# Kernel optimization log

Measured on AMD Instinct MI355X. Metric: run time of the kernel, lower is better.

The kernel has to match this reference:

```python
import jax, jax.numpy as jnp
import numpy as np

K = 6                 # color-coding parameter; K-1 message-passing steps
N = 50000             # num nodes
E = 1600000           # num edges (avg degree 32)
F = 384               # num_node_features = K * 2**K


def setup_inputs() -> dict:
    key = jax.random.key(0)
    k1, k2, k3, k4, k5 = jax.random.split(key, 5)
    s = 1.0 / np.sqrt(F)
    x = jax.random.normal(k1, (N, F), dtype=jnp.float32)
    edge_index = jax.random.randint(k2, (2, E), 0, N, dtype=jnp.int32)
    batch = jnp.zeros((N,), dtype=jnp.int32)  # unused by forward, kept for signature parity
    W_rel = jax.random.normal(k3, (F, F), dtype=jnp.float32) * s   # GraphConv lin_rel weight
    W_root = jax.random.normal(k4, (F, F), dtype=jnp.float32) * s  # GraphConv lin_root weight
    W_lin = jax.random.normal(k5, (1, F), dtype=jnp.float32) * s   # readout linear (no bias)
    return {"x": x, "edge_index": edge_index, "batch": batch,
            "W_rel": W_rel, "W_root": W_root, "W_lin": W_lin}


def reference(x, edge_index, batch, W_rel, W_root, W_lin):
    src = edge_index[0]
    dst = edge_index[1]
    # K-1 iterations of PyG GraphConv(aggr='add', bias=False) + relu:
    #   out = segment_sum(x[src] -> dst) @ W_rel^T + x @ W_root^T
    for _ in range(K - 1):
        agg = jax.ops.segment_sum(x[src], dst, num_segments=N)  # [N, F]
        x = jax.nn.relu(agg @ W_rel.T + x @ W_root.T)
    # readout: Linear(F, 1, bias=False)
    return x @ W_lin.T  # [N, 1]
```

## Files before the change

kernel.cpp:

```cpp
#include <hip/hip_runtime.h>
#include <hip/hip_bf16.h>

#define NN 50000
#define EE 1600000
#define FF 384
#define MPAD 50048
#define NITER 5
#define EPB 6250
#define BCAP 220000
#define GRP 6250

typedef unsigned int u32;
typedef unsigned short u16;
typedef __attribute__((ext_vector_type(8))) short short8;
typedef __attribute__((ext_vector_type(4))) float f32x4;

typedef const __attribute__((address_space(1))) void* gptr_t;
typedef __attribute__((address_space(3))) void* lptr_t;

__device__ __forceinline__ float bf_lo(u32 u) {
  u32 v = u << 16;
  return __builtin_bit_cast(float, v);
}
__device__ __forceinline__ float bf_hi(u32 u) {
  u32 v = u & 0xFFFF0000u;
  return __builtin_bit_cast(float, v);
}
__device__ __forceinline__ u32 f2bf(float f) {
  u32 u = __builtin_bit_cast(u32, f);
  return (u + 0x7FFFu + ((u >> 16) & 1u)) >> 16;
}
__device__ __forceinline__ u32 pack2(float lo, float hi) {
  return f2bf(lo) | (f2bf(hi) << 16);
}
__device__ __forceinline__ void load16_lds(const void* g, void* l) {
  __builtin_amdgcn_global_load_lds((gptr_t)g, (lptr_t)l, 16, 0, 0);
}

__global__ void init_bcur_kernel(int* __restrict__ bcur) {
  if (threadIdx.x < 8) bcur[threadIdx.x] = threadIdx.x * BCAP;
}

__global__ __launch_bounds__(256) void bucket_scatter_kernel(
    const int* __restrict__ src, const int* __restrict__ dst,
    int* __restrict__ bcur, int* __restrict__ es_src, int* __restrict__ es_dst) {
  __shared__ int osrc[EPB];
  __shared__ int odst[EPB];
  __shared__ int h[8], lo8[8], gbase[8], c2[8];
  const int t = threadIdx.x;
  if (t < 8) { h[t] = 0; c2[t] = 0; }
  __syncthreads();
  const int e0 = blockIdx.x * EPB;
  for (int i = t; i < EPB; i += 256) {
    int d = dst[e0 + i];
    atomicAdd(&h[d / GRP], 1);
  }
  __syncthreads();
  if (t == 0) { int r = 0; for (int b = 0; b < 8; ++b) { lo8[b] = r; r += h[b]; } }
  __syncthreads();
  if (t < 8) gbase[t] = atomicAdd(&bcur[t], h[t]);
  __syncthreads();
  for (int i = t; i < EPB; i += 256) {
    int s = src[e0 + i], d = dst[e0 + i];
    int b = d / GRP;
    int p = lo8[b] + atomicAdd(&c2[b], 1);
    osrc[p] = s; odst[p] = d;
  }
  __syncthreads();
  for (int i = t; i < EPB; i += 256) {
    int b = 0;
    while (b < 7 && i >= lo8[b + 1]) ++b;
    int g = gbase[b] + (i - lo8[b]);
    es_src[g] = osrc[i];
    es_dst[g] = odst[i];
  }
}

__global__ __launch_bounds__(256) void hist3_kernel(
    const int* __restrict__ es_dst, const int* __restrict__ bcur,
    int* __restrict__ cnt) {
  const int g = blockIdx.x & 7;
  const int sub = blockIdx.x >> 3;
  const int base = g * BCAP;
  const int n = bcur[g] - base;
  const int chunk = (n + 31) >> 5;
  const int i0 = sub * chunk;
  int i1 = i0 + chunk; if (i1 > n) i1 = n;
  for (int i = i0 + threadIdx.x; i < i1; i += 256)
    atomicAdd(&cnt[es_dst[base + i]], 1);
}

__global__ void scan_kernel(const int* __restrict__ cnt, int* __restrict__ row_start,
                            int* __restrict__ cursor) {
  __shared__ int wsum[4];
  const int CH = 196;
  int t = threadIdx.x;
  int lo = t * CH;
  int hi = lo + CH; if (hi > NN) hi = NN;
  int s = 0;
  int n4 = (hi - lo) >> 2;
  const int4* p = (const int4*)(cnt + lo);
  for (int i = 0; i < n4; ++i) { int4 c = p[i]; s += c.x + c.y + c.z + c.w; }
  int lane = t & 63, w = t >> 6;
  int v = s;
  for (int d = 1; d < 64; d <<= 1) { int u = __shfl_up(v, d, 64); if (lane >= d) v += u; }
  if (lane == 63) wsum[w] = v;
  __syncthreads();
  int run = v - s;
  for (int i = 0; i < w; ++i) run += wsum[i];
  int4* q1 = (int4*)(row_start + lo);
  int4* q2 = (int4*)(cursor + lo);
  for (int k = 0; k < n4; ++k) {
    int4 c = p[k];
    int4 o; o.x = run; o.y = run + c.x; o.z = o.y + c.y; o.w = o.z + c.z;
    run = o.w + c.w;
    q1[k] = o; q2[k] = o;
  }
  if (hi == NN && lo < NN) row_start[NN] = run;
}

__global__ __launch_bounds__(256) void scatter3_kernel(
    const int* __restrict__ es_src, const int* __restrict__ es_dst,
    const int* __restrict__ bcur, int* __restrict__ cursor, int* __restrict__ col) {
  const int g = blockIdx.x & 7;
  const int sub = blockIdx.x >> 3;
  const int base = g * BCAP;
  const int n = bcur[g] - base;
  const int chunk = (n + 31) >> 5;
  const int i0 = sub * chunk;
  int i1 = i0 + chunk; if (i1 > n) i1 = n;
  for (int i = i0 + threadIdx.x; i < i1; i += 256) {
    int d = es_dst[base + i];
    int s = es_src[base + i];
    int p = atomicAdd(&cursor[d], 1);
    col[p] = s;
  }
}

__global__ void convert_x_kernel(const float* __restrict__ xin, u16* __restrict__ xout) {
  size_t i = ((size_t)blockIdx.x * 256 + threadIdx.x) * 4;
  if (i >= (size_t)NN * FF) return;
  float4 f = *(const float4*)(xin + i);
  u32 o0 = pack2(f.x, f.y);
  u32 o1 = pack2(f.z, f.w);
  u32* q = (u32*)(xout + i);
  q[0] = o0; q[1] = o1;
}

__global__ void build_bt_kernel(const float* __restrict__ Wr, const float* __restrict__ Wt,
                                u16* __restrict__ Bt) {
  int i = blockIdx.x * 256 + threadIdx.x;
  if (i >= FF * 2 * FF) return;
  int n = i / (2 * FF);
  int k = i - n * (2 * FF);
  float v = (k < FF) ? Wr[n * FF + k] : Wt[n * FF + (k - FF)];
  Bt[i] = (u16)f2bf(v);
}

__global__ void spmm_pass_kernel(const u16* __restrict__ x, const int* __restrict__ rs,
                                 const int* __restrict__ col, u16* __restrict__ agg,
                                 const int fo) {
  int row = blockIdx.x * 4 + (threadIdx.x >> 6);
  int lane = threadIdx.x & 63;
  if (row >= NN) return;
  int j0 = rs[row], j1 = rs[row + 1];
  float alo = 0.f, ahi = 0.f;
  const u32* xw = (const u32*)x + fo + lane;
  int j = j0;
  for (; j + 8 <= j1; j += 8) {
    int s0 = col[j + 0], s1 = col[j + 1], s2 = col[j + 2], s3 = col[j + 3];
    int s4 = col[j + 4], s5 = col[j + 5], s6 = col[j + 6], s7 = col[j + 7];
    u32 u0 = xw[(size_t)s0 * 192];
    u32 u1 = xw[(size_t)s1 * 192];
    u32 u2 = xw[(size_t)s2 * 192];
    u32 u3 = xw[(size_t)s3 * 192];
    u32 u4 = xw[(size_t)s4 * 192];
    u32 u5 = xw[(size_t)s5 * 192];
    u32 u6 = xw[(size_t)s6 * 192];
    u32 u7 = xw[(size_t)s7 * 192];
    alo += bf_lo(u0) + bf_lo(u1) + bf_lo(u2) + bf_lo(u3) +
           bf_lo(u4) + bf_lo(u5) + bf_lo(u6) + bf_lo(u7);
    ahi += bf_hi(u0) + bf_hi(u1) + bf_hi(u2) + bf_hi(u3) +
           bf_hi(u4) + bf_hi(u5) + bf_hi(u6) + bf_hi(u7);
  }
  for (; j < j1; ++j) {
    u32 u = xw[(size_t)col[j] * 192];
    alo += bf_lo(u); ahi += bf_hi(u);
  }
  ((u32*)agg)[(size_t)row * 192 + fo + lane] = pack2(alo, ahi);
}

__global__ __launch_bounds__(512, 4) void gemm_kernel(
    const u16* __restrict__ Aagg, const u16* __restrict__ Ax,
    const u16* __restrict__ Bt, u16* __restrict__ Xout) {
  __shared__ __align__(16) u16 As[2][64 * 64];
  __shared__ __align__(16) u16 Bs[384 * 64];

  const int orig = blockIdx.x;
  const int xcd = orig & 7, idx = orig >> 3;
  const int wg = ((xcd < 6) ? xcd * 98 : 6 * 98 + (xcd - 6) * 97) + idx;
  const int m0 = wg * 64;

  const int tid = threadIdx.x;
  const int lane = tid & 63;
  const int w = tid >> 6;
  const int wr = w >> 2;
  const int wc = w & 3;

  f32x4 acc[2][6] = {};

#define STAGE_A(KT, BUF)                                                        \
  {                                                                             \
    const u16* Asrc_ = ((KT) < 6) ? Aagg : Ax;                                  \
    const int kbA_ = (((KT) < 6) ? (KT) : (KT)-6) << 7;                         \
    const int rA_ = tid >> 3;                                                   \
    const int bcA_ = (tid & 7) << 4;                                            \
    load16_lds((const char*)Asrc_ + (size_t)(m0 + rA_) * 768 + kbA_ +           \
                   (bcA_ ^ ((rA_ & 7) << 4)),                                   \
               (char*)&As[BUF][0] + tid * 16);                                  \
  }

#define STAGE_B(KT)                                                             \
  {                                                                             \
    const int kbB_ = (KT) << 7;                                                 \
    _Pragma("unroll")                                                           \
    for (int i = 0; i < 6; ++i) {                                               \
      const int c = tid + i * 512;                                              \
      const int rB_ = c >> 3;                                                   \
      const int bcB_ = (c & 7) << 4;                                            \
      load16_lds((const char*)Bt + (size_t)rB_ * 1536 + kbB_ +                  \
                     (bcB_ ^ ((rB_ & 7) << 4)),                                 \
                 (char*)&Bs[0] + c * 16);                                       \
    }                                                                           \
  }

  STAGE_A(0, 0);
  STAGE_B(0);
  __syncthreads();

  int buf = 0;
  for (int kt = 0; kt < 12; ++kt) {
    if (kt < 11) STAGE_A(kt + 1, buf ^ 1);
#pragma unroll
    for (int ks = 0; ks < 2; ++ks) {
      short8 af[2], bfm[6];
#pragma unroll
      for (int ni = 0; ni < 6; ++ni) {
        const int r = wc * 96 + ni * 16 + (lane & 15);
        const int bc = (ks * 64 + ((lane >> 4) << 4)) ^ ((r & 7) << 4);
        bfm[ni] = *(const short8*)((const char*)&Bs[0] + r * 128 + bc);
      }
#pragma unroll
      for (int mi = 0; mi < 2; ++mi) {
        const int r = wr * 32 + mi * 16 + (lane & 15);
        const int bc = (ks * 64 + ((lane >> 4) << 4)) ^ ((r & 7) << 4);
        af[mi] = *(const short8*)((const char*)&As[buf][0] + r * 128 + bc);
      }
#pragma unroll
      for (int mi = 0; mi < 2; ++mi)
#pragma unroll
        for (int ni = 0; ni < 6; ++ni)
          acc[mi][ni] = __builtin_amdgcn_mfma_f32_16x16x32_bf16(af[mi], bfm[ni], acc[mi][ni], 0, 0, 0);
    }
    __syncthreads();
    if (kt < 11) {
      STAGE_B(kt + 1);
      __syncthreads();
    }
    buf ^= 1;
  }

#pragma unroll
  for (int mi = 0; mi < 2; ++mi) {
#pragma unroll
    for (int r = 0; r < 4; ++r) {
      const int row = m0 + wr * 32 + mi * 16 + ((lane >> 4) << 2) + r;
      u16* orow = Xout + (size_t)row * FF + wc * 96 + (lane & 15);
#pragma unroll
      for (int ni = 0; ni < 6; ++ni) {
        float v = fmaxf(acc[mi][ni][r], 0.0f);
        orow[ni * 16] = (u16)f2bf(v);
      }
    }
  }
#undef STAGE_A
#undef STAGE_B
}

__global__ void readout_kernel(const u16* __restrict__ x, const float* __restrict__ wl,
                               float* __restrict__ out) {
  int row = blockIdx.x * 4 + (threadIdx.x >> 6);
  int lane = threadIdx.x & 63;
  if (row >= NN) return;
  const u32* p = (const u32*)(x + (size_t)row * FF) + lane * 3;
  u32 u0 = p[0], u1 = p[1], u2 = p[2];
  const float* w = wl + lane * 6;
  float s = bf_lo(u0) * w[0] + bf_hi(u0) * w[1] +
            bf_lo(u1) * w[2] + bf_hi(u1) * w[3] +
            bf_lo(u2) * w[4] + bf_hi(u2) * w[5];
#pragma unroll
  for (int off = 32; off > 0; off >>= 1) s += __shfl_down(s, off, 64);
  if (lane == 0) out[row] = s;
}

extern "C" void kernel_launch(void* const* d_in, const int* in_sizes, int n_in,
                              void* d_out, int out_size, void* d_ws, size_t ws_size,
                              hipStream_t stream) {
  const float* x_in = (const float*)d_in[0];
  const int* ei = (const int*)d_in[1];
  const float* W_rel = (const float*)d_in[3];
  const float* W_root = (const float*)d_in[4];
  const float* W_lin = (const float*)d_in[5];
  float* out = (float*)d_out;

  char* ws = (char*)d_ws;
  int* cnt = (int*)(ws);
  int* bcur = cnt + NN;
  int* row_start = (int*)(ws + 200064);
  int* cursor = (int*)(ws + 400128);
  int* col = (int*)(ws + 600192);
  u16* Bt = (u16*)(ws + 7000192);
  u16* agg = (u16*)(ws + 7590016);
  u16* x0 = (u16*)(ws + 46026880);
  u16* x1 = (u16*)(ws + 84463744);
  if (ws_size < (size_t)122900608) return;
  int* es_src = (int*)(ws + 7590016);
  int* es_dst = (int*)(ws + 7590016 + 7040000);

  const int* esrc = ei;
  const int* edst = ei + EE;

  hipMemsetAsync(cnt, 0, NN * sizeof(int), stream);
  hipMemsetAsync(agg + (size_t)NN * FF, 0, (size_t)(MPAD - NN) * FF * sizeof(u16), stream);
  hipMemsetAsync(x0 + (size_t)NN * FF, 0, (size_t)(MPAD - NN) * FF * sizeof(u16), stream);
  hipMemsetAsync(x1 + (size_t)NN * FF, 0, (size_t)(MPAD - NN) * FF * sizeof(u16), stream);

  init_bcur_kernel<<<1, 64, 0, stream>>>(bcur);
  bucket_scatter_kernel<<<EE / EPB, 256, 0, stream>>>(esrc, edst, bcur, es_src, es_dst);
  hist3_kernel<<<256, 256, 0, stream>>>(es_dst, bcur, cnt);
  scan_kernel<<<1, 256, 0, stream>>>(cnt, row_start, cursor);
  scatter3_kernel<<<256, 256, 0, stream>>>(es_src, es_dst, bcur, cursor, col);
  convert_x_kernel<<<(NN * FF / 4 + 255) / 256, 256, 0, stream>>>(x_in, x0);
  build_bt_kernel<<<(FF * 2 * FF + 255) / 256, 256, 0, stream>>>(W_rel, W_root, Bt);

  u16* xs = x0;
  u16* xd = x1;
  for (int t = 0; t < NITER; ++t) {
    for (int p = 0; p < 3; ++p)
      spmm_pass_kernel<<<NN / 4, 256, 0, stream>>>(xs, row_start, col, agg, p * 64);
    gemm_kernel<<<MPAD / 64, 512, 0, stream>>>(agg, xs, Bt, xd);
    u16* tmp = xs; xs = xd; xd = tmp;
  }
  readout_kernel<<<NN / 4, 256, 0, stream>>>(xs, W_lin, out);
}
```

Baseline: 1.238 ms.

## Replace global atomic histogram and scatter with per-block LDS partial histograms

The CSR build now has each block histogram its slice of a destination bucket into shared memory and write the result as a partial count array. A reduce kernel turns those partials into per-block exclusive offsets and per-node totals. The scatter then places edges using cursors held in shared memory instead of global atomics on a cursor array. This removes contended global atomics from preprocessing, at the cost of an extra kernel launch and extra partial-array traffic.

```diff
diff --git a/kernel.cpp b/kernel.cpp
--- a/kernel.cpp
+++ b/kernel.cpp
@@ -76,22 +76,43 @@
   }
 }
 
-__global__ __launch_bounds__(256) void hist3_kernel(
+__global__ __launch_bounds__(256) void hist_part_kernel(
     const int* __restrict__ es_dst, const int* __restrict__ bcur,
-    int* __restrict__ cnt) {
-  const int g = blockIdx.x & 7;
-  const int sub = blockIdx.x >> 3;
+    int* __restrict__ part) {
+  __shared__ int h[GRP];
+  const int g = blockIdx.x >> 5;
+  const int s = blockIdx.x & 31;
+  const int lo = g * GRP;
   const int base = g * BCAP;
   const int n = bcur[g] - base;
   const int chunk = (n + 31) >> 5;
-  const int i0 = sub * chunk;
+  const int i0 = s * chunk;
   int i1 = i0 + chunk; if (i1 > n) i1 = n;
+  for (int i = threadIdx.x; i < GRP; i += 256) h[i] = 0;
+  __syncthreads();
   for (int i = i0 + threadIdx.x; i < i1; i += 256)
-    atomicAdd(&cnt[es_dst[base + i]], 1);
-}
-
-__global__ void scan_kernel(const int* __restrict__ cnt, int* __restrict__ row_start,
-                            int* __restrict__ cursor) {
+    atomicAdd(&h[es_dst[base + i] - lo], 1);
+  __syncthreads();
+  int* po = part + (size_t)blockIdx.x * GRP;
+  for (int i = threadIdx.x; i < GRP; i += 256) po[i] = h[i];
+}
+
+__global__ void reduce_kernel(int* __restrict__ part, int* __restrict__ cnt) {
+  int r = blockIdx.x * 256 + threadIdx.x;
+  if (r >= NN) return;
+  int g = r / GRP, o = r - g * GRP;
+  int* p = part + (size_t)(g * 32) * GRP + o;
+  int run = 0;
+#pragma unroll
+  for (int s = 0; s < 32; ++s) {
+    int v = p[(size_t)s * GRP];
+    p[(size_t)s * GRP] = run;
+    run += v;
+  }
+  cnt[r] = run;
+}
+
+__global__ void scan_kernel(const int* __restrict__ cnt, int* __restrict__ row_start) {
   __shared__ int wsum[4];
   const int CH = 196;
   int t = threadIdx.x;
@@ -109,31 +130,36 @@
   int run = v - s;
   for (int i = 0; i < w; ++i) run += wsum[i];
   int4* q1 = (int4*)(row_start + lo);
-  int4* q2 = (int4*)(cursor + lo);
   for (int k = 0; k < n4; ++k) {
     int4 c = p[k];
     int4 o; o.x = run; o.y = run + c.x; o.z = o.y + c.y; o.w = o.z + c.z;
     run = o.w + c.w;
-    q1[k] = o; q2[k] = o;
+    q1[k] = o;
   }
   if (hi == NN && lo < NN) row_start[NN] = run;
 }
 
-__global__ __launch_bounds__(256) void scatter3_kernel(
+__global__ __launch_bounds__(256) void scatter4_kernel(
     const int* __restrict__ es_src, const int* __restrict__ es_dst,
-    const int* __restrict__ bcur, int* __restrict__ cursor, int* __restrict__ col) {
-  const int g = blockIdx.x & 7;
-  const int sub = blockIdx.x >> 3;
+    const int* __restrict__ bcur, const int* __restrict__ row_start,
+    const int* __restrict__ part, int* __restrict__ col) {
+  __shared__ int cur[GRP];
+  const int g = blockIdx.x >> 5;
+  const int s = blockIdx.x & 31;
+  const int lo = g * GRP;
   const int base = g * BCAP;
   const int n = bcur[g] - base;
   const int chunk = (n + 31) >> 5;
-  const int i0 = sub * chunk;
+  const int i0 = s * chunk;
   int i1 = i0 + chunk; if (i1 > n) i1 = n;
+  const int* po = part + (size_t)blockIdx.x * GRP;
+  for (int i = threadIdx.x; i < GRP; i += 256)
+    cur[i] = row_start[lo + i] + po[i];
+  __syncthreads();
   for (int i = i0 + threadIdx.x; i < i1; i += 256) {
     int d = es_dst[base + i];
-    int s = es_src[base + i];
-    int p = atomicAdd(&cursor[d], 1);
-    col[p] = s;
+    int p = atomicAdd(&cur[d - lo], 1);
+    col[p] = es_src[base + i];
   }
 }
 
@@ -317,7 +343,6 @@
   int* cnt = (int*)(ws);
   int* bcur = cnt + NN;
   int* row_start = (int*)(ws + 200064);
-  int* cursor = (int*)(ws + 400128);
   int* col = (int*)(ws + 600192);
   u16* Bt = (u16*)(ws + 7000192);
   u16* agg = (u16*)(ws + 7590016);
@@ -326,20 +351,21 @@
   if (ws_size < (size_t)122900608) return;
   int* es_src = (int*)(ws + 7590016);
   int* es_dst = (int*)(ws + 7590016 + 7040000);
+  int* part = (int*)(ws + 7590016 + 14080000);
 
   const int* esrc = ei;
   const int* edst = ei + EE;
 
-  hipMemsetAsync(cnt, 0, NN * sizeof(int), stream);
   hipMemsetAsync(agg + (size_t)NN * FF, 0, (size_t)(MPAD - NN) * FF * sizeof(u16), stream);
   hipMemsetAsync(x0 + (size_t)NN * FF, 0, (size_t)(MPAD - NN) * FF * sizeof(u16), stream);
   hipMemsetAsync(x1 + (size_t)NN * FF, 0, (size_t)(MPAD - NN) * FF * sizeof(u16), stream);
 
   init_bcur_kernel<<<1, 64, 0, stream>>>(bcur);
   bucket_scatter_kernel<<<EE / EPB, 256, 0, stream>>>(esrc, edst, bcur, es_src, es_dst);
-  hist3_kernel<<<256, 256, 0, stream>>>(es_dst, bcur, cnt);
-  scan_kernel<<<1, 256, 0, stream>>>(cnt, row_start, cursor);
-  scatter3_kernel<<<256, 256, 0, stream>>>(es_src, es_dst, bcur, cursor, col);
+  hist_part_kernel<<<256, 256, 0, stream>>>(es_dst, bcur, part);
+  reduce_kernel<<<(NN + 255) / 256, 256, 0, stream>>>(part, cnt);
+  scan_kernel<<<1, 256, 0, stream>>>(cnt, row_start);
+  scatter4_kernel<<<256, 256, 0, stream>>>(es_src, es_dst, bcur, row_start, part, col);
   convert_x_kernel<<<(NN * FF / 4 + 255) / 256, 256, 0, stream>>>(x_in, x0);
   build_bt_kernel<<<(FF * 2 * FF + 255) / 256, 256, 0, stream>>>(W_rel, W_root, Bt);
 
```

After: 1.133 ms, median of 2. 1.09x faster.
